# Kernel tuning notes

Measured on AMD Instinct MI355X. Metric: run time of the kernel, lower is better.

## Reference

```python
import jax, jax.numpy as jnp
import numpy as np

A_MIN = 0.001
EPS = 1e-08


def setup_inputs() -> dict:
    key = jax.random.key(0)
    k1, k2, k3, k4 = jax.random.split(key, 4)
    B, O, I = 512, 1024, 512
    x = jax.random.normal(k1, (B, I), dtype=jnp.float32)
    translation = jax.random.uniform(k2, (O, I), dtype=jnp.float32, minval=-1.0, maxval=1.0)
    scale_raw = jax.random.uniform(k3, (O, I), dtype=jnp.float32, minval=-2.0, maxval=0.0)
    weights = jax.random.normal(k4, (O, I), dtype=jnp.float32) * (1.0 / np.sqrt(I))
    return {"x": x, "translation": translation, "scale_raw": scale_raw, "weights": weights}


def reference(x, translation, scale_raw, weights):
    # x: (B, I); params: (O, I)
    scale = A_MIN + jax.nn.softplus(scale_raw)  # (O, I)
    # s: (B, O, I) broadcast intermediate
    s = (x[:, None, :] - translation[None, :, :]) / (scale[None, :, :] + EPS)
    s2 = s * s
    wavelet = (1.0 - s2) * jnp.exp(-0.5 * s2)  # mexican hat
    y = jnp.einsum('oi,boi->bo', weights, wavelet)  # reduce over in_features
    return y
```

## Files before the change

### kernel.cpp

```cpp
#include <hip/hip_runtime.h>
#include <hip/hip_bf16.h>


#define WL_A_MIN 0.001f
#define WL_EPS   1e-8f

constexpr int WL_B = 512;
constexpr int WL_O = 1024;
constexpr int WL_I = 512;

#define WL_SQK  0.84932180553704583800f
#define WL_IK   1.38629436111989061883f
#define WL_L2E  1.44269504088896340736f
#define WL_LN2  0.69314718055994530942f

typedef float v2f __attribute__((ext_vector_type(2)));

struct P3 { float nti, inv, w; };

__device__ __forceinline__ float fast_exp2(float a) {
#if __has_builtin(__builtin_amdgcn_exp2f)
    return __builtin_amdgcn_exp2f(a);
#else
    return exp2f(a);
#endif
}
__device__ __forceinline__ float fast_log2(float a) {
#if __has_builtin(__builtin_amdgcn_logf)
    return __builtin_amdgcn_logf(a);
#else
    return __log2f(a);
#endif
}
__device__ __forceinline__ float fast_rcp(float a) {
#if __has_builtin(__builtin_amdgcn_rcpf)
    return __builtin_amdgcn_rcpf(a);
#else
    return 1.0f / a;
#endif
}

__global__ __launch_bounds__(256) void wl_prep(
    const float* __restrict__ translation,
    const float* __restrict__ scale_raw,
    const float* __restrict__ weights,
    P3* __restrict__ pT3)
{
    const int lane   = threadIdx.x & 63;
    const int ic     = threadIdx.x >> 6;
    const int o      = blockIdx.x * 64 + lane;
    const int i_base = blockIdx.y * 64 + ic * 16;

    #pragma unroll 4
    for (int k = 0; k < 16; ++k) {
        int i  = i_base + k;
        int gi = o * WL_I + i;
        float t  = translation[gi];
        float sr = scale_raw[gi];
        float w  = weights[gi];
        float ex    = fast_exp2(sr * WL_L2E);
        float sp    = fast_log2(1.0f + ex) * WL_LN2;
        float inv   = fast_rcp(WL_A_MIN + sp + WL_EPS);
        float inv_s = inv * WL_SQK;
        P3 pv; pv.nti = -t * inv_s; pv.inv = inv_s; pv.w = w;
        pT3[(size_t)i * WL_O + o] = pv;
    }
}

__global__ __launch_bounds__(512, 4) void wl_main(
    const float* __restrict__ x,
    const P3* __restrict__ pT3,
    float* __restrict__ out)
{
    __shared__ float smem[WL_I * 16];

    const int tid  = threadIdx.x;
    const int lane = tid & 63;
    const int wid  = tid >> 6;
    const int o    = blockIdx.x * 64 + lane;
    const int b0   = blockIdx.y * 16;

    {
        const int b_l = tid & 15;
        const int seg = tid >> 4;
        const float* xg = &x[(b0 + b_l) * WL_I + seg * 16];
        #pragma unroll
        for (int q = 0; q < 4; ++q) {
            float4 v = *reinterpret_cast<const float4*>(xg + q * 4);
            int i0 = seg * 16 + q * 4;
            smem[(i0 + 0) * 16 + b_l] = v.x;
            smem[(i0 + 1) * 16 + b_l] = v.y;
            smem[(i0 + 2) * 16 + b_l] = v.z;
            smem[(i0 + 3) * 16 + b_l] = v.w;
        }
    }
    __syncthreads();

    const int oct = wid & 1;
    const int iq  = wid >> 1;
    const P3*    pp   = pT3 + o;
    const float* xrow = &smem[oct * 8];

    v2f aE0 = {0.f,0.f}, aE1 = {0.f,0.f}, aE2 = {0.f,0.f}, aE3 = {0.f,0.f};
    v2f aU0 = {0.f,0.f}, aU1 = {0.f,0.f}, aU2 = {0.f,0.f}, aU3 = {0.f,0.f};

    const int iBeg = iq * 128;
    #pragma unroll 4
    for (int ii = 0; ii < 128; ++ii) {
        const int i = iBeg + ii;
        P3 p = pp[(size_t)i * WL_O];
        float4 xa = *reinterpret_cast<const float4*>(xrow + i * 16);
        float4 xb = *reinterpret_cast<const float4*>(xrow + i * 16 + 4);

        v2f nti = {p.nti, p.nti};
        v2f inv = {p.inv, p.inv};
        v2f wv  = {p.w,  p.w};

        v2f x01 = {xa.x, xa.y};
        v2f x23 = {xa.z, xa.w};
        v2f x45 = {xb.x, xb.y};
        v2f x67 = {xb.z, xb.w};

        v2f s0 = __builtin_elementwise_fma(x01, inv, nti);
        v2f s1 = __builtin_elementwise_fma(x23, inv, nti);
        v2f s2 = __builtin_elementwise_fma(x45, inv, nti);
        v2f s3 = __builtin_elementwise_fma(x67, inv, nti);
        v2f u0 = s0 * s0;
        v2f u1 = s1 * s1;
        v2f u2 = s2 * s2;
        v2f u3 = s3 * s3;
        v2f e0 = {fast_exp2(-u0.x), fast_exp2(-u0.y)};
        v2f e1 = {fast_exp2(-u1.x), fast_exp2(-u1.y)};
        v2f e2 = {fast_exp2(-u2.x), fast_exp2(-u2.y)};
        v2f e3 = {fast_exp2(-u3.x), fast_exp2(-u3.y)};
        aE0 = __builtin_elementwise_fma(wv, e0, aE0);
        aE1 = __builtin_elementwise_fma(wv, e1, aE1);
        aE2 = __builtin_elementwise_fma(wv, e2, aE2);
        aE3 = __builtin_elementwise_fma(wv, e3, aE3);
        v2f ue0 = u0 * e0;
        v2f ue1 = u1 * e1;
        v2f ue2 = u2 * e2;
        v2f ue3 = u3 * e3;
        aU0 = __builtin_elementwise_fma(wv, ue0, aU0);
        aU1 = __builtin_elementwise_fma(wv, ue1, aU1);
        aU2 = __builtin_elementwise_fma(wv, ue2, aU2);
        aU3 = __builtin_elementwise_fma(wv, ue3, aU3);
    }

    __syncthreads();
    constexpr int RS = 20;
    if (iq != 0) {
        float4* dst = reinterpret_cast<float4*>(
            &smem[(((iq - 1) * 2 + oct) * 64 + lane) * RS]);
        dst[0] = make_float4(aE0.x, aE0.y, aE1.x, aE1.y);
        dst[1] = make_float4(aE2.x, aE2.y, aE3.x, aE3.y);
        dst[2] = make_float4(aU0.x, aU0.y, aU1.x, aU1.y);
        dst[3] = make_float4(aU2.x, aU2.y, aU3.x, aU3.y);
    }
    __syncthreads();
    if (iq == 0) {
        float E[8] = {aE0.x, aE0.y, aE1.x, aE1.y, aE2.x, aE2.y, aE3.x, aE3.y};
        float U[8] = {aU0.x, aU0.y, aU1.x, aU1.y, aU2.x, aU2.y, aU3.x, aU3.y};
        #pragma unroll
        for (int q = 1; q < 4; ++q) {
            const float4* src = reinterpret_cast<const float4*>(
                &smem[(((q - 1) * 2 + oct) * 64 + lane) * RS]);
            float4 v0 = src[0], v1 = src[1], v2 = src[2], v3 = src[3];
            E[0] += v0.x; E[1] += v0.y; E[2] += v0.z; E[3] += v0.w;
            E[4] += v1.x; E[5] += v1.y; E[6] += v1.z; E[7] += v1.w;
            U[0] += v2.x; U[1] += v2.y; U[2] += v2.z; U[3] += v2.w;
            U[4] += v3.x; U[5] += v3.y; U[6] += v3.z; U[7] += v3.w;
        }
        const int b = b0 + oct * 8;
        #pragma unroll
        for (int k = 0; k < 8; ++k)
            out[(size_t)(b + k) * WL_O + o] = fmaf(-WL_IK, U[k], E[k]);
    }
}

extern "C" void kernel_launch(void* const* d_in, const int* in_sizes, int n_in,
                              void* d_out, int out_size, void* d_ws, size_t ws_size,
                              hipStream_t stream) {
    const float* x           = (const float*)d_in[0];
    const float* translation = (const float*)d_in[1];
    const float* scale_raw   = (const float*)d_in[2];
    const float* weights     = (const float*)d_in[3];
    float*       out         = (float*)d_out;
    P3*          pT3         = (P3*)d_ws;

    wl_prep<<<dim3(WL_O / 64, WL_I / 64), dim3(256), 0, stream>>>(
        translation, scale_raw, weights, pT3);

    wl_main<<<dim3(WL_O / 64, WL_B / 16), dim3(512), 0, stream>>>(
        x, pT3, out);
}
```

Baseline: 111.9 us.

## Shrink batch tile to 8, split reduction over 8 waves, XCD-aware block mapping

```diff
diff --git a/kernel.cpp b/kernel.cpp
--- a/kernel.cpp
+++ b/kernel.cpp
@@ -67,50 +67,52 @@
     }
 }
 
-__global__ __launch_bounds__(512, 4) void wl_main(
+__global__ __launch_bounds__(512, 8) void wl_main(
     const float* __restrict__ x,
     const P3* __restrict__ pT3,
     float* __restrict__ out)
 {
-    __shared__ float smem[WL_I * 16];
+    __shared__ float smem[WL_I * 8];
 
     const int tid  = threadIdx.x;
     const int lane = tid & 63;
     const int wid  = tid >> 6;
-    const int o    = blockIdx.x * 64 + lane;
-    const int b0   = blockIdx.y * 16;
+    const int bid  = blockIdx.x;
+    const int xcd  = bid & 7;
+    const int slot = bid >> 3;
+    const int o    = (xcd * 2 + (slot & 1)) * 64 + lane;
+    const int b0   = (slot >> 1) * 8;
 
     {
-        const int b_l = tid & 15;
-        const int seg = tid >> 4;
-        const float* xg = &x[(b0 + b_l) * WL_I + seg * 16];
-        #pragma unroll
-        for (int q = 0; q < 4; ++q) {
-            float4 v = *reinterpret_cast<const float4*>(xg + q * 4);
-            int i0 = seg * 16 + q * 4;
-            smem[(i0 + 0) * 16 + b_l] = v.x;
-            smem[(i0 + 1) * 16 + b_l] = v.y;
-            smem[(i0 + 2) * 16 + b_l] = v.z;
-            smem[(i0 + 3) * 16 + b_l] = v.w;
-        }
-    }
-    __syncthreads();
-
-    const int oct = wid & 1;
-    const int iq  = wid >> 1;
-    const P3*    pp   = pT3 + o;
-    const float* xrow = &smem[oct * 8];
+        const int b_l = tid & 7;
+        const int seg = tid >> 3;
+        const float* xg = &x[(b0 + b_l) * WL_I + seg * 8];
+        float4 v0 = *reinterpret_cast<const float4*>(xg);
+        float4 v1 = *reinterpret_cast<const float4*>(xg + 4);
+        int a0 = (seg * 8) * 8 + b_l;
+        smem[a0 + 0 * 8] = v0.x;
+        smem[a0 + 1 * 8] = v0.y;
+        smem[a0 + 2 * 8] = v0.z;
+        smem[a0 + 3 * 8] = v0.w;
+        smem[a0 + 4 * 8] = v1.x;
+        smem[a0 + 5 * 8] = v1.y;
+        smem[a0 + 6 * 8] = v1.z;
+        smem[a0 + 7 * 8] = v1.w;
+    }
+    __syncthreads();
+
+    const P3* pp = pT3 + o;
 
     v2f aE0 = {0.f,0.f}, aE1 = {0.f,0.f}, aE2 = {0.f,0.f}, aE3 = {0.f,0.f};
     v2f aU0 = {0.f,0.f}, aU1 = {0.f,0.f}, aU2 = {0.f,0.f}, aU3 = {0.f,0.f};
 
-    const int iBeg = iq * 128;
-    #pragma unroll 4
-    for (int ii = 0; ii < 128; ++ii) {
+    const int iBeg = wid * 64;
+    #pragma unroll 8
+    for (int ii = 0; ii < 64; ++ii) {
         const int i = iBeg + ii;
         P3 p = pp[(size_t)i * WL_O];
-        float4 xa = *reinterpret_cast<const float4*>(xrow + i * 16);
-        float4 xb = *reinterpret_cast<const float4*>(xrow + i * 16 + 4);
+        float4 xa = *reinterpret_cast<const float4*>(&smem[i * 8]);
+        float4 xb = *reinterpret_cast<const float4*>(&smem[i * 8 + 4]);
 
         v2f nti = {p.nti, p.nti};
         v2f inv = {p.inv, p.inv};
@@ -147,34 +149,63 @@
         aU3 = __builtin_elementwise_fma(wv, ue3, aU3);
     }
 
-    __syncthreads();
-    constexpr int RS = 20;
-    if (iq != 0) {
-        float4* dst = reinterpret_cast<float4*>(
-            &smem[(((iq - 1) * 2 + oct) * 64 + lane) * RS]);
-        dst[0] = make_float4(aE0.x, aE0.y, aE1.x, aE1.y);
-        dst[1] = make_float4(aE2.x, aE2.y, aE3.x, aE3.y);
-        dst[2] = make_float4(aU0.x, aU0.y, aU1.x, aU1.y);
-        dst[3] = make_float4(aU2.x, aU2.y, aU3.x, aU3.y);
-    }
-    __syncthreads();
-    if (iq == 0) {
-        float E[8] = {aE0.x, aE0.y, aE1.x, aE1.y, aE2.x, aE2.y, aE3.x, aE3.y};
-        float U[8] = {aU0.x, aU0.y, aU1.x, aU1.y, aU2.x, aU2.y, aU3.x, aU3.y};
-        #pragma unroll
-        for (int q = 1; q < 4; ++q) {
-            const float4* src = reinterpret_cast<const float4*>(
-                &smem[(((q - 1) * 2 + oct) * 64 + lane) * RS]);
-            float4 v0 = src[0], v1 = src[1], v2 = src[2], v3 = src[3];
-            E[0] += v0.x; E[1] += v0.y; E[2] += v0.z; E[3] += v0.w;
-            E[4] += v1.x; E[5] += v1.y; E[6] += v1.z; E[7] += v1.w;
-            U[0] += v2.x; U[1] += v2.y; U[2] += v2.z; U[3] += v2.w;
-            U[4] += v3.x; U[5] += v3.y; U[6] += v3.z; U[7] += v3.w;
-        }
-        const int b = b0 + oct * 8;
+    float E[8] = {aE0.x, aE0.y, aE1.x, aE1.y, aE2.x, aE2.y, aE3.x, aE3.y};
+    float U[8] = {aU0.x, aU0.y, aU1.x, aU1.y, aU2.x, aU2.y, aU3.x, aU3.y};
+
+    __syncthreads();
+    float4* s4 = reinterpret_cast<float4*>(smem);
+    if (wid >= 4) {
+        float4* d = &s4[((wid - 4) * 64 + lane) * 4];
+        d[0] = make_float4(E[0], E[1], E[2], E[3]);
+        d[1] = make_float4(E[4], E[5], E[6], E[7]);
+        d[2] = make_float4(U[0], U[1], U[2], U[3]);
+        d[3] = make_float4(U[4], U[5], U[6], U[7]);
+    }
+    __syncthreads();
+    if (wid < 4) {
+        const float4* sv = &s4[(wid * 64 + lane) * 4];
+        float4 a = sv[0], b = sv[1], c = sv[2], d = sv[3];
+        E[0] += a.x; E[1] += a.y; E[2] += a.z; E[3] += a.w;
+        E[4] += b.x; E[5] += b.y; E[6] += b.z; E[7] += b.w;
+        U[0] += c.x; U[1] += c.y; U[2] += c.z; U[3] += c.w;
+        U[4] += d.x; U[5] += d.y; U[6] += d.z; U[7] += d.w;
+    }
+    __syncthreads();
+    if (wid == 2 || wid == 3) {
+        float4* d = &s4[((wid - 2) * 64 + lane) * 4];
+        d[0] = make_float4(E[0], E[1], E[2], E[3]);
+        d[1] = make_float4(E[4], E[5], E[6], E[7]);
+        d[2] = make_float4(U[0], U[1], U[2], U[3]);
+        d[3] = make_float4(U[4], U[5], U[6], U[7]);
+    }
+    __syncthreads();
+    if (wid < 2) {
+        const float4* sv = &s4[(wid * 64 + lane) * 4];
+        float4 a = sv[0], b = sv[1], c = sv[2], d = sv[3];
+        E[0] += a.x; E[1] += a.y; E[2] += a.z; E[3] += a.w;
+        E[4] += b.x; E[5] += b.y; E[6] += b.z; E[7] += b.w;
+        U[0] += c.x; U[1] += c.y; U[2] += c.z; U[3] += c.w;
+        U[4] += d.x; U[5] += d.y; U[6] += d.z; U[7] += d.w;
+    }
+    __syncthreads();
+    if (wid == 1) {
+        float4* d = &s4[lane * 4];
+        d[0] = make_float4(E[0], E[1], E[2], E[3]);
+        d[1] = make_float4(E[4], E[5], E[6], E[7]);
+        d[2] = make_float4(U[0], U[1], U[2], U[3]);
+        d[3] = make_float4(U[4], U[5], U[6], U[7]);
+    }
+    __syncthreads();
+    if (wid == 0) {
+        const float4* sv = &s4[lane * 4];
+        float4 a = sv[0], b = sv[1], c = sv[2], d = sv[3];
+        E[0] += a.x; E[1] += a.y; E[2] += a.z; E[3] += a.w;
+        E[4] += b.x; E[5] += b.y; E[6] += b.z; E[7] += b.w;
+        U[0] += c.x; U[1] += c.y; U[2] += c.z; U[3] += c.w;
+        U[4] += d.x; U[5] += d.y; U[6] += d.z; U[7] += d.w;
         #pragma unroll
         for (int k = 0; k < 8; ++k)
-            out[(size_t)(b + k) * WL_O + o] = fmaf(-WL_IK, U[k], E[k]);
+            out[(size_t)(b0 + k) * WL_O + o] = fmaf(-WL_IK, U[k], E[k]);
     }
 }
 
@@ -191,6 +222,5 @@
     wl_prep<<<dim3(WL_O / 64, WL_I / 64), dim3(256), 0, stream>>>(
         translation, scale_raw, weights, pT3);
 
-    wl_main<<<dim3(WL_O / 64, WL_B / 16), dim3(512), 0, stream>>>(
-        x, pT3, out);
-}
+    wl_main<<<dim3(1024), dim3(512), 0, stream>>>(x, pT3, out);
+}
```

Result: slower. 171.8 us (+53.5%).

## Shrink main-kernel batch tile to 4 rows with 256-thread blocks

Applied to the files above, without the earlier changes.

```diff
diff --git a/kernel.cpp b/kernel.cpp
--- a/kernel.cpp
+++ b/kernel.cpp
@@ -67,114 +67,90 @@
     }
 }
 
-__global__ __launch_bounds__(512, 4) void wl_main(
+constexpr int R_REG = 544;
+constexpr int R_KS  = 68;
+
+__global__ __launch_bounds__(256, 6) void wl_main(
     const float* __restrict__ x,
     const P3* __restrict__ pT3,
     float* __restrict__ out)
 {
-    __shared__ float smem[WL_I * 16];
+    __shared__ float smem[4 * R_REG];
 
     const int tid  = threadIdx.x;
     const int lane = tid & 63;
     const int wid  = tid >> 6;
     const int o    = blockIdx.x * 64 + lane;
-    const int b0   = blockIdx.y * 16;
+    const int b0   = blockIdx.y * 4;
 
-    {
-        const int b_l = tid & 15;
-        const int seg = tid >> 4;
-        const float* xg = &x[(b0 + b_l) * WL_I + seg * 16];
-        #pragma unroll
-        for (int q = 0; q < 4; ++q) {
-            float4 v = *reinterpret_cast<const float4*>(xg + q * 4);
-            int i0 = seg * 16 + q * 4;
-            smem[(i0 + 0) * 16 + b_l] = v.x;
-            smem[(i0 + 1) * 16 + b_l] = v.y;
-            smem[(i0 + 2) * 16 + b_l] = v.z;
-            smem[(i0 + 3) * 16 + b_l] = v.w;
-        }
+    #pragma unroll
+    for (int c = 0; c < 2; ++c) {
+        int i = c * 256 + tid;
+        float4 v;
+        v.x = x[(size_t)(b0 + 0) * WL_I + i];
+        v.y = x[(size_t)(b0 + 1) * WL_I + i];
+        v.z = x[(size_t)(b0 + 2) * WL_I + i];
+        v.w = x[(size_t)(b0 + 3) * WL_I + i];
+        *reinterpret_cast<float4*>(&smem[i * 4]) = v;
     }
     __syncthreads();
 
-    const int oct = wid & 1;
-    const int iq  = wid >> 1;
-    const P3*    pp   = pT3 + o;
-    const float* xrow = &smem[oct * 8];
+    const P3* pp = pT3 + o;
 
-    v2f aE0 = {0.f,0.f}, aE1 = {0.f,0.f}, aE2 = {0.f,0.f}, aE3 = {0.f,0.f};
-    v2f aU0 = {0.f,0.f}, aU1 = {0.f,0.f}, aU2 = {0.f,0.f}, aU3 = {0.f,0.f};
+    v2f aE0 = {0.f, 0.f}, aE1 = {0.f, 0.f};
+    v2f aU0 = {0.f, 0.f}, aU1 = {0.f, 0.f};
 
-    const int iBeg = iq * 128;
+    const int iBeg = wid * 128;
     #pragma unroll 4
     for (int ii = 0; ii < 128; ++ii) {
         const int i = iBeg + ii;
         P3 p = pp[(size_t)i * WL_O];
-        float4 xa = *reinterpret_cast<const float4*>(xrow + i * 16);
-        float4 xb = *reinterpret_cast<const float4*>(xrow + i * 16 + 4);
+        float4 xq = *reinterpret_cast<const float4*>(&smem[i * 4]);
 
         v2f nti = {p.nti, p.nti};
         v2f inv = {p.inv, p.inv};
         v2f wv  = {p.w,  p.w};
 
-        v2f x01 = {xa.x, xa.y};
-        v2f x23 = {xa.z, xa.w};
-        v2f x45 = {xb.x, xb.y};
-        v2f x67 = {xb.z, xb.w};
+        v2f x01 = {xq.x, xq.y};
+        v2f x23 = {xq.z, xq.w};
 
         v2f s0 = __builtin_elementwise_fma(x01, inv, nti);
         v2f s1 = __builtin_elementwise_fma(x23, inv, nti);
-        v2f s2 = __builtin_elementwise_fma(x45, inv, nti);
-        v2f s3 = __builtin_elementwise_fma(x67, inv, nti);
         v2f u0 = s0 * s0;
         v2f u1 = s1 * s1;
-        v2f u2 = s2 * s2;
-        v2f u3 = s3 * s3;
         v2f e0 = {fast_exp2(-u0.x), fast_exp2(-u0.y)};
         v2f e1 = {fast_exp2(-u1.x), fast_exp2(-u1.y)};
-        v2f e2 = {fast_exp2(-u2.x), fast_exp2(-u2.y)};
-        v2f e3 = {fast_exp2(-u3.x), fast_exp2(-u3.y)};
         aE0 = __builtin_elementwise_fma(wv, e0, aE0);
         aE1 = __builtin_elementwise_fma(wv, e1, aE1);
-        aE2 = __builtin_elementwise_fma(wv, e2, aE2);
-        aE3 = __builtin_elementwise_fma(wv, e3, aE3);
         v2f ue0 = u0 * e0;
         v2f ue1 = u1 * e1;
-        v2f ue2 = u2 * e2;
-        v2f ue3 = u3 * e3;
         aU0 = __builtin_elementwise_fma(wv, ue0, aU0);
         aU1 = __builtin_elementwise_fma(wv, ue1, aU1);
-        aU2 = __builtin_elementwise_fma(wv, ue2, aU2);
-        aU3 = __builtin_elementwise_fma(wv, ue3, aU3);
     }
 
     __syncthreads();
-    constexpr int RS = 20;
-    if (iq != 0) {
-        float4* dst = reinterpret_cast<float4*>(
-            &smem[(((iq - 1) * 2 + oct) * 64 + lane) * RS]);
-        dst[0] = make_float4(aE0.x, aE0.y, aE1.x, aE1.y);
-        dst[1] = make_float4(aE2.x, aE2.y, aE3.x, aE3.y);
-        dst[2] = make_float4(aU0.x, aU0.y, aU1.x, aU1.y);
-        dst[3] = make_float4(aU2.x, aU2.y, aU3.x, aU3.y);
+    {
+        float* r = &smem[wid * R_REG + lane];
+        r[0 * R_KS] = aE0.x; r[1 * R_KS] = aE0.y;
+        r[2 * R_KS] = aE1.x; r[3 * R_KS] = aE1.y;
+        r[4 * R_KS] = aU0.x; r[5 * R_KS] = aU0.y;
+        r[6 * R_KS] = aU1.x; r[7 * R_KS] = aU1.y;
     }
     __syncthreads();
-    if (iq == 0) {
-        float E[8] = {aE0.x, aE0.y, aE1.x, aE1.y, aE2.x, aE2.y, aE3.x, aE3.y};
-        float U[8] = {aU0.x, aU0.y, aU1.x, aU1.y, aU2.x, aU2.y, aU3.x, aU3.y};
+    if (wid == 0) {
+        float E[4] = {0.f, 0.f, 0.f, 0.f};
+        float U[4] = {0.f, 0.f, 0.f, 0.f};
         #pragma unroll
-        for (int q = 1; q < 4; ++q) {
-            const float4* src = reinterpret_cast<const float4*>(
-                &smem[(((q - 1) * 2 + oct) * 64 + lane) * RS]);
-            float4 v0 = src[0], v1 = src[1], v2 = src[2], v3 = src[3];
-            E[0] += v0.x; E[1] += v0.y; E[2] += v0.z; E[3] += v0.w;
-            E[4] += v1.x; E[5] += v1.y; E[6] += v1.z; E[7] += v1.w;
-            U[0] += v2.x; U[1] += v2.y; U[2] += v2.z; U[3] += v2.w;
-            U[4] += v3.x; U[5] += v3.y; U[6] += v3.z; U[7] += v3.w;
+        for (int w = 0; w < 4; ++w) {
+            const float* r = &smem[w * R_REG + lane];
+            E[0] += r[0 * R_KS]; E[1] += r[1 * R_KS];
+            E[2] += r[2 * R_KS]; E[3] += r[3 * R_KS];
+            U[0] += r[4 * R_KS]; U[1] += r[5 * R_KS];
+            U[2] += r[6 * R_KS]; U[3] += r[7 * R_KS];
         }
-        const int b = b0 + oct * 8;
         #pragma unroll
-        for (int k = 0; k < 8; ++k)
-            out[(size_t)(b + k) * WL_O + o] = fmaf(-WL_IK, U[k], E[k]);
+        for (int k = 0; k < 4; ++k)
+            out[(size_t)(b0 + k) * WL_O + o] = fmaf(-WL_IK, U[k], E[k]);
     }
 }
 
@@ -191,6 +167,5 @@
     wl_prep<<<dim3(WL_O / 64, WL_I / 64), dim3(256), 0, stream>>>(
         translation, scale_raw, weights, pT3);
 
-    wl_main<<<dim3(WL_O / 64, WL_B / 16), dim3(512), 0, stream>>>(
-        x, pT3, out);
+    wl_main<<<dim3(WL_O / 64, WL_B / 4), dim3(256), 0, stream>>>(x, pT3, out);
 }
```

Result: slower. 114.6 us (+2.4%).
